# Performance work log

Hardware: AMD Instinct MI355X
Metric: run time of the kernel (lower is better)

Reference implementation:

```python
import jax, jax.numpy as jnp
import numpy as np

B, P, S, D = 256, 40, 60, 64


def setup_inputs() -> dict:
    key = jax.random.key(0)
    ks = jax.random.split(key, 12)
    sc = 1.0 / np.sqrt(D)
    return {
        "x": jax.random.normal(ks[0], (B, P, S, D), dtype=jnp.float32),
        "Wq": jax.random.normal(ks[1], (D, D), dtype=jnp.float32) * sc,
        "bq": jnp.zeros((D,), dtype=jnp.float32),
        "Wk": jax.random.normal(ks[2], (D, D), dtype=jnp.float32) * sc,
        "bk": jnp.zeros((D,), dtype=jnp.float32),
        "Wv": jax.random.normal(ks[3], (D, D), dtype=jnp.float32) * sc,
        "bv": jnp.zeros((D,), dtype=jnp.float32),
        "W1": jax.random.normal(ks[4], (D, D), dtype=jnp.float32) * sc,
        "b1": jnp.zeros((D,), dtype=jnp.float32),
        "W2": jax.random.normal(ks[5], (D, D), dtype=jnp.float32) * sc,
        "b2": jnp.zeros((D,), dtype=jnp.float32),
        "W3": jax.random.normal(ks[6], (1, D), dtype=jnp.float32) * sc,
        "b3": jnp.zeros((1,), dtype=jnp.float32),
    }


def reference(x, Wq, bq, Wk, bk, Wv, bv, W1, b1, W2, b2, W3, b3):
    # x: [B, P, S, D]; fully vectorized version of the per-batch torch loop
    q = jnp.einsum("bpsd,ed->bpse", x, Wq) + bq
    k = jnp.einsum("bpsd,ed->bpse", x, Wk) + bk
    v = jnp.einsum("bpsd,ed->bpse", x, Wv) + bv
    scores = jnp.einsum("bpqd,bpkd->bpqk", q, k) / jnp.sqrt(jnp.float32(D))
    attn = jax.nn.softmax(scores, axis=-1)
    weighted = jnp.einsum("bpqk,bpkd->bpqd", attn, v)  # [B,P,S,D]
    h = jax.nn.relu(jnp.einsum("bpsd,ed->bpse", weighted, W1) + b1)
    h = jax.nn.relu(jnp.einsum("bpsd,ed->bpse", h, W2) + b2)
    out = jnp.einsum("bpsd,od->bpso", h, W3) + b3  # [B,P,S,1]
    return out[..., 0]  # [B, P, S] == (B, NUM_PARTS, 60)
```

## Files before the change

kernel.cpp:

```cpp
#include <hip/hip_runtime.h>
#include <math.h>


typedef _Float16 half8 __attribute__((ext_vector_type(8)));
typedef __fp16 fp16x2 __attribute__((ext_vector_type(2)));
typedef float f4 __attribute__((ext_vector_type(4)));

#define MFMA16(a, b, c) __builtin_amdgcn_mfma_f32_16x16x32_f16((a), (b), (c), 0, 0, 0)

__global__ __launch_bounds__(256) void prep_weights(
    const float* __restrict__ Wq, const float* __restrict__ Wk,
    const float* __restrict__ Wv, const float* __restrict__ W1,
    const float* __restrict__ W2, _Float16* __restrict__ wsH) {
    int idx = blockIdx.x * 256 + threadIdx.x;
    int m = idx >> 12, r = idx & 4095;
    const float* src = (m == 0) ? Wq : (m == 1) ? Wk : (m == 2) ? Wv
                        : (m == 3) ? W1 : W2;
    float v;
    if (m < 3) {
        v = src[r];
    } else {
        int e = r >> 6, kp = r & 63;
        int ks = kp >> 5, gg = (kp >> 3) & 3, i = kp & 7;
        int d = 16 * (2 * ks + (i >> 2)) + 4 * gg + (i & 3);
        v = src[e * 64 + d];
    }
    wsH[idx] = (_Float16)v;
}

__device__ __forceinline__ half8 pk8(f4 a, f4 b) {
    union { half8 h; fp16x2 p[4]; } u;
    u.p[0] = __builtin_amdgcn_cvt_pkrtz(a[0], a[1]);
    u.p[1] = __builtin_amdgcn_cvt_pkrtz(a[2], a[3]);
    u.p[2] = __builtin_amdgcn_cvt_pkrtz(b[0], b[1]);
    u.p[3] = __builtin_amdgcn_cvt_pkrtz(b[2], b[3]);
    return u.h;
}

#define GEMM_H(AEXPR, BEXPR, CEXPR)                                          \
    do {                                                                     \
        _Pragma("unroll")                                                    \
        for (int ks = 0; ks < 2; ++ks) {                                     \
            half8 afr[4], bfr[2];                                            \
            _Pragma("unroll")                                                \
            for (int t = 0; t < 4; ++t) afr[t] = (AEXPR);                    \
            _Pragma("unroll")                                                \
            for (int nb = 0; nb < 2; ++nb) {                                 \
                const int nt = 2 * h + nb; (void)nt;                         \
                bfr[nb] = (BEXPR);                                           \
            }                                                                \
            _Pragma("unroll")                                                \
            for (int mt = 0; mt < 4; ++mt)                                   \
                _Pragma("unroll")                                            \
                for (int nb = 0; nb < 2; ++nb) {                             \
                    const int nt = 2 * h + nb; (void)nt;                     \
                    acc2[mt][nb] = MFMA16(afr[mt], bfr[nb],                  \
                                          ks == 0 ? (CEXPR) : acc2[mt][nb]); \
                }                                                            \
        }                                                                    \
    } while (0)

#define MKFR_H(dst, RELU)                                                    \
    do {                                                                     \
        _Pragma("unroll")                                                    \
        for (int nb = 0; nb < 2; ++nb)                                       \
            _Pragma("unroll")                                                \
            for (int ks = 0; ks < 2; ++ks) {                                 \
                f4 a_ = acc2[2 * ks][nb], b_ = acc2[2 * ks + 1][nb];         \
                if (RELU) {                                                  \
                    _Pragma("unroll")                                        \
                    for (int j = 0; j < 4; ++j) {                            \
                        a_[j] = fmaxf(a_[j], 0.f);                           \
                        b_[j] = fmaxf(b_[j], 0.f);                           \
                    }                                                        \
                }                                                            \
                dst[2 * h + nb][ks] = pk8(a_, b_);                           \
            }                                                                \
    } while (0)

#define WFRAG(widx, RB) (*(const half8*)&wlds[(widx) * 4096 + (16 * (RB) + lo) * 64 + \
                                              ((32 * ks + 8 * g) ^ ((lo & 7) << 3))])

#define XFRAG(RB) __extension__({                                            \
    int row_ = 16 * (RB) + lo;                                               \
    int rowc_ = row_ < 60 ? row_ : 48;                                       \
    half8 v_ = *(const half8*)&wlds[xbase + rowc_ * 64 +                     \
                                    ((32 * ks + 8 * g) ^ ((lo & 7) << 3))];  \
    if (row_ >= 60) { half8 z_ = {}; v_ = z_; }                              \
    v_; })

__global__ __launch_bounds__(512, 1) void fused_f16(
    const float* __restrict__ x, const _Float16* __restrict__ wH,
    const float* __restrict__ bq, const float* __restrict__ bk,
    const float* __restrict__ bv, const float* __restrict__ b1,
    const float* __restrict__ b2, const float* __restrict__ W3,
    const float* __restrict__ b3, float* __restrict__ out) {
    __shared__ __align__(16) _Float16 wlds[51200];

    const int tid = threadIdx.x;
    const int l = tid & 63;
    const int w = tid >> 6;
    const int lo = l & 15, g = l >> 4;

    #pragma unroll
    for (int rep = 0; rep < 5; ++rep) {
        int chunk = rep * 512 + tid;
        int widx = chunk >> 9;
        int rem = chunk & 511;
        int row = rem >> 3, c = rem & 7;
        *(half8*)&wlds[widx * 4096 + row * 64 + ((c * 8) ^ ((row & 7) << 3))] =
            *(const half8*)&wH[widx * 4096 + row * 64 + c * 8];
    }
    __syncthreads();

    const int part = blockIdx.x * 8 + w;
    const int xbase = 20480 + w * 3840;
    const float* __restrict__ xp = x + (size_t)part * (60 * 64);

    #pragma unroll
    for (int m = 0; m < 8; ++m) {
        int chunk = m * 64 + l;
        if (chunk < 480) {
            int row = chunk >> 3, c = chunk & 7;
            const float* p = xp + row * 64 + c * 8;
            half8 hv = pk8(*(const f4*)p, *(const f4*)(p + 4));
            *(half8*)&wlds[xbase + row * 64 + ((c * 8) ^ ((row & 7) << 3))] = hv;
        }
    }

    const f4 zc = {0.f, 0.f, 0.f, 0.f};
    f4 acc2[4][2];
    f4 brow[4];
    half8 qf[4][2], kf[4][2], vf[4][2], pf[4][2], wtf[4][2], h1f[4][2];

    #pragma unroll
    for (int mt = 0; mt < 4; ++mt) brow[mt] = *(const f4*)&bq[16 * mt + 4 * g];
    #pragma unroll
    for (int h = 0; h < 2; ++h) {
        GEMM_H(WFRAG(0, t), XFRAG(nt), brow[mt]);
        MKFR_H(qf, false);
    }

    #pragma unroll
    for (int mt = 0; mt < 4; ++mt) brow[mt] = *(const f4*)&bk[16 * mt + 4 * g];
    #pragma unroll
    for (int h = 0; h < 2; ++h) {
        GEMM_H(WFRAG(1, t), XFRAG(nt), brow[mt]);
        MKFR_H(kf, false);
    }

    #pragma unroll
    for (int h = 0; h < 2; ++h) {
        GEMM_H(kf[t][ks], qf[nt][ks], zc);
        #pragma unroll
        for (int nb = 0; nb < 2; ++nb) {
            float sum = 0.f;
            #pragma unroll
            for (int mt = 0; mt < 4; ++mt)
                #pragma unroll
                for (int j = 0; j < 4; ++j) {
                    float e = (mt == 3 && g == 3)
                                  ? 0.f
                                  : exp2f(acc2[mt][nb][j] * 0.1803368801111137f);
                    acc2[mt][nb][j] = e;
                    sum += e;
                }
            sum += __shfl_xor(sum, 16);
            sum += __shfl_xor(sum, 32);
            float inv = 1.f / sum;
            #pragma unroll
            for (int mt = 0; mt < 4; ++mt)
                #pragma unroll
                for (int j = 0; j < 4; ++j) acc2[mt][nb][j] *= inv;
        }
        MKFR_H(pf, false);
    }

    #pragma unroll
    for (int h = 0; h < 2; ++h) {
        float bc[2];
        #pragma unroll
        for (int nb = 0; nb < 2; ++nb) bc[nb] = bv[16 * (2 * h + nb) + lo];
        GEMM_H(XFRAG(t), WFRAG(2, nt),
               ((f4){bc[nb], bc[nb], bc[nb], bc[nb]}));
        MKFR_H(vf, false);
    }

    #pragma unroll
    for (int h = 0; h < 2; ++h) {
        GEMM_H(vf[t][ks], pf[nt][ks], zc);
        MKFR_H(wtf, false);
    }

    #pragma unroll
    for (int mt = 0; mt < 4; ++mt) brow[mt] = *(const f4*)&b1[16 * mt + 4 * g];
    #pragma unroll
    for (int h = 0; h < 2; ++h) {
        GEMM_H(WFRAG(3, t), wtf[nt][ks], brow[mt]);
        MKFR_H(h1f, true);
    }

    #pragma unroll
    for (int mt = 0; mt < 4; ++mt) brow[mt] = *(const f4*)&b2[16 * mt + 4 * g];
    f4 w3r[4];
    #pragma unroll
    for (int mt = 0; mt < 4; ++mt) w3r[mt] = *(const f4*)&W3[16 * mt + 4 * g];
    float b3v = b3[0];
    #pragma unroll
    for (int h = 0; h < 2; ++h) {
        GEMM_H(WFRAG(4, t), h1f[nt][ks], brow[mt]);
        #pragma unroll
        for (int nb = 0; nb < 2; ++nb) {
            float sres = 0.f;
            #pragma unroll
            for (int mt = 0; mt < 4; ++mt)
                #pragma unroll
                for (int j = 0; j < 4; ++j)
                    sres += fmaxf(acc2[mt][nb][j], 0.f) * w3r[mt][j];
            sres += __shfl_xor(sres, 16);
            sres += __shfl_xor(sres, 32);
            if (g == 0) {
                int s = 16 * (2 * h + nb) + lo;
                if (s < 60) out[(size_t)part * 60 + s] = sres + b3v;
            }
        }
    }
}

extern "C" void kernel_launch(void* const* d_in, const int* in_sizes, int n_in,
                              void* d_out, int out_size, void* d_ws, size_t ws_size,
                              hipStream_t stream) {
    const float* x  = (const float*)d_in[0];
    const float* Wq = (const float*)d_in[1];
    const float* bq = (const float*)d_in[2];
    const float* Wk = (const float*)d_in[3];
    const float* bk = (const float*)d_in[4];
    const float* Wv = (const float*)d_in[5];
    const float* bv = (const float*)d_in[6];
    const float* W1 = (const float*)d_in[7];
    const float* b1 = (const float*)d_in[8];
    const float* W2 = (const float*)d_in[9];
    const float* b2 = (const float*)d_in[10];
    const float* W3 = (const float*)d_in[11];
    const float* b3 = (const float*)d_in[12];
    _Float16* wsH = (_Float16*)d_ws;

    prep_weights<<<80, 256, 0, stream>>>(Wq, Wk, Wv, W1, W2, wsH);
    fused_f16<<<1280, 512, 0, stream>>>(x, wsH, bq, bk, bv, b1, b2, W3, b3,
                                        (float*)d_out);
}
```

Measured before the change: 69.92 us.

## Process two parts per wavefront to amortize weight loading and halve grid

Each wavefront now handles two (batch,part) slices instead of one, interleaving their MFMA chains so the two independent streams give instruction-level parallelism. The grid is halved to 640 blocks, so the per-block LDS weight staging is amortized over twice the work. LDS grows to 160KB and register pressure roughly doubles, which risks spills and leaves fewer blocks in flight on 256 CUs (640 blocks is about 2.5 waves).

Result: slower. 74.89 us (+7.1%).

```diff
diff --git a/kernel.cpp b/kernel.cpp
--- a/kernel.cpp
+++ b/kernel.cpp
@@ -37,7 +37,7 @@
     return u.h;
 }
 
-#define GEMM_H(AEXPR, BEXPR, CEXPR)                                          \
+#define GEMM_H(ACC, AEXPR, BEXPR, CEXPR)                                     \
     do {                                                                     \
         _Pragma("unroll")                                                    \
         for (int ks = 0; ks < 2; ++ks) {                                     \
@@ -54,19 +54,19 @@
                 _Pragma("unroll")                                            \
                 for (int nb = 0; nb < 2; ++nb) {                             \
                     const int nt = 2 * h + nb; (void)nt;                     \
-                    acc2[mt][nb] = MFMA16(afr[mt], bfr[nb],                  \
-                                          ks == 0 ? (CEXPR) : acc2[mt][nb]); \
+                    ACC[mt][nb] = MFMA16(afr[mt], bfr[nb],                   \
+                                         ks == 0 ? (CEXPR) : ACC[mt][nb]);   \
                 }                                                            \
         }                                                                    \
     } while (0)
 
-#define MKFR_H(dst, RELU)                                                    \
+#define MKFR_H(dst, ACC, RELU)                                               \
     do {                                                                     \
         _Pragma("unroll")                                                    \
         for (int nb = 0; nb < 2; ++nb)                                       \
             _Pragma("unroll")                                                \
             for (int ks = 0; ks < 2; ++ks) {                                 \
-                f4 a_ = acc2[2 * ks][nb], b_ = acc2[2 * ks + 1][nb];         \
+                f4 a_ = ACC[2 * ks][nb], b_ = ACC[2 * ks + 1][nb];           \
                 if (RELU) {                                                  \
                     _Pragma("unroll")                                        \
                     for (int j = 0; j < 4; ++j) {                            \
@@ -81,10 +81,10 @@
 #define WFRAG(widx, RB) (*(const half8*)&wlds[(widx) * 4096 + (16 * (RB) + lo) * 64 + \
                                               ((32 * ks + 8 * g) ^ ((lo & 7) << 3))])
 
-#define XFRAG(RB) __extension__({                                            \
+#define XFRAG(XB, RB) __extension__({                                        \
     int row_ = 16 * (RB) + lo;                                               \
     int rowc_ = row_ < 60 ? row_ : 48;                                       \
-    half8 v_ = *(const half8*)&wlds[xbase + rowc_ * 64 +                     \
+    half8 v_ = *(const half8*)&wlds[(XB) + rowc_ * 64 +                      \
                                     ((32 * ks + 8 * g) ^ ((lo & 7) << 3))];  \
     if (row_ >= 60) { half8 z_ = {}; v_ = z_; }                              \
     v_; })
@@ -95,7 +95,7 @@
     const float* __restrict__ bv, const float* __restrict__ b1,
     const float* __restrict__ b2, const float* __restrict__ W3,
     const float* __restrict__ b3, float* __restrict__ out) {
-    __shared__ __align__(16) _Float16 wlds[51200];
+    __shared__ __align__(16) _Float16 wlds[81920];
 
     const int tid = threadIdx.x;
     const int l = tid & 63;
@@ -113,92 +113,114 @@
     }
     __syncthreads();
 
-    const int part = blockIdx.x * 8 + w;
-    const int xbase = 20480 + w * 3840;
-    const float* __restrict__ xp = x + (size_t)part * (60 * 64);
-
-    #pragma unroll
-    for (int m = 0; m < 8; ++m) {
-        int chunk = m * 64 + l;
-        if (chunk < 480) {
-            int row = chunk >> 3, c = chunk & 7;
-            const float* p = xp + row * 64 + c * 8;
-            half8 hv = pk8(*(const f4*)p, *(const f4*)(p + 4));
-            *(half8*)&wlds[xbase + row * 64 + ((c * 8) ^ ((row & 7) << 3))] = hv;
+    const int pr0 = blockIdx.x * 16 + w * 2;
+    const int xb0 = 20480 + (2 * w + 0) * 3840;
+    const int xb1 = 20480 + (2 * w + 1) * 3840;
+
+    #pragma unroll
+    for (int P = 0; P < 2; ++P) {
+        const float* __restrict__ xp = x + (size_t)(pr0 + P) * (60 * 64);
+        const int XB = P ? xb1 : xb0;
+        #pragma unroll
+        for (int m = 0; m < 8; ++m) {
+            int chunk = m * 64 + l;
+            if (chunk < 480) {
+                int row = chunk >> 3, c = chunk & 7;
+                const float* p = xp + row * 64 + c * 8;
+                half8 hv = pk8(*(const f4*)p, *(const f4*)(p + 4));
+                *(half8*)&wlds[XB + row * 64 + ((c * 8) ^ ((row & 7) << 3))] = hv;
+            }
         }
     }
 
     const f4 zc = {0.f, 0.f, 0.f, 0.f};
-    f4 acc2[4][2];
+    f4 acc2[2][4][2];
     f4 brow[4];
-    half8 qf[4][2], kf[4][2], vf[4][2], pf[4][2], wtf[4][2], h1f[4][2];
+    half8 qf[2][4][2], kf[2][4][2], vf[2][4][2], pf[2][4][2], wtf[2][4][2],
+          h1f[2][4][2];
 
     #pragma unroll
     for (int mt = 0; mt < 4; ++mt) brow[mt] = *(const f4*)&bq[16 * mt + 4 * g];
     #pragma unroll
-    for (int h = 0; h < 2; ++h) {
-        GEMM_H(WFRAG(0, t), XFRAG(nt), brow[mt]);
-        MKFR_H(qf, false);
-    }
+    for (int h = 0; h < 2; ++h)
+        #pragma unroll
+        for (int P = 0; P < 2; ++P) {
+            const int XB = P ? xb1 : xb0;
+            GEMM_H(acc2[P], WFRAG(0, t), XFRAG(XB, nt), brow[mt]);
+            MKFR_H(qf[P], acc2[P], false);
+        }
 
     #pragma unroll
     for (int mt = 0; mt < 4; ++mt) brow[mt] = *(const f4*)&bk[16 * mt + 4 * g];
     #pragma unroll
-    for (int h = 0; h < 2; ++h) {
-        GEMM_H(WFRAG(1, t), XFRAG(nt), brow[mt]);
-        MKFR_H(kf, false);
-    }
-
-    #pragma unroll
-    for (int h = 0; h < 2; ++h) {
-        GEMM_H(kf[t][ks], qf[nt][ks], zc);
-        #pragma unroll
-        for (int nb = 0; nb < 2; ++nb) {
-            float sum = 0.f;
+    for (int h = 0; h < 2; ++h)
+        #pragma unroll
+        for (int P = 0; P < 2; ++P) {
+            const int XB = P ? xb1 : xb0;
+            GEMM_H(acc2[P], WFRAG(1, t), XFRAG(XB, nt), brow[mt]);
+            MKFR_H(kf[P], acc2[P], false);
+        }
+
+    #pragma unroll
+    for (int h = 0; h < 2; ++h)
+        #pragma unroll
+        for (int P = 0; P < 2; ++P) {
+            GEMM_H(acc2[P], kf[P][t][ks], qf[P][nt][ks], zc);
             #pragma unroll
-            for (int mt = 0; mt < 4; ++mt)
+            for (int nb = 0; nb < 2; ++nb) {
+                float sum = 0.f;
                 #pragma unroll
-                for (int j = 0; j < 4; ++j) {
-                    float e = (mt == 3 && g == 3)
-                                  ? 0.f
-                                  : exp2f(acc2[mt][nb][j] * 0.1803368801111137f);
-                    acc2[mt][nb][j] = e;
-                    sum += e;
-                }
-            sum += __shfl_xor(sum, 16);
-            sum += __shfl_xor(sum, 32);
-            float inv = 1.f / sum;
+                for (int mt = 0; mt < 4; ++mt)
+                    #pragma unroll
+                    for (int j = 0; j < 4; ++j) {
+                        float e = (mt == 3 && g == 3)
+                                      ? 0.f
+                                      : exp2f(acc2[P][mt][nb][j] *
+                                              0.1803368801111137f);
+                        acc2[P][mt][nb][j] = e;
+                        sum += e;
+                    }
+                sum += __shfl_xor(sum, 16);
+                sum += __shfl_xor(sum, 32);
+                float inv = 1.f / sum;
+                #pragma unroll
+                for (int mt = 0; mt < 4; ++mt)
+                    #pragma unroll
+                    for (int j = 0; j < 4; ++j) acc2[P][mt][nb][j] *= inv;
+            }
+            MKFR_H(pf[P], acc2[P], false);
+        }
+
+    #pragma unroll
+    for (int h = 0; h < 2; ++h)
+        #pragma unroll
+        for (int P = 0; P < 2; ++P) {
+            const int XB = P ? xb1 : xb0;
+            float bc[2];
             #pragma unroll
-            for (int mt = 0; mt < 4; ++mt)
-                #pragma unroll
-                for (int j = 0; j < 4; ++j) acc2[mt][nb][j] *= inv;
-        }
-        MKFR_H(pf, false);
-    }
-
-    #pragma unroll
-    for (int h = 0; h < 2; ++h) {
-        float bc[2];
-        #pragma unroll
-        for (int nb = 0; nb < 2; ++nb) bc[nb] = bv[16 * (2 * h + nb) + lo];
-        GEMM_H(XFRAG(t), WFRAG(2, nt),
-               ((f4){bc[nb], bc[nb], bc[nb], bc[nb]}));
-        MKFR_H(vf, false);
-    }
-
-    #pragma unroll
-    for (int h = 0; h < 2; ++h) {
-        GEMM_H(vf[t][ks], pf[nt][ks], zc);
-        MKFR_H(wtf, false);
-    }
+            for (int nb = 0; nb < 2; ++nb) bc[nb] = bv[16 * (2 * h + nb) + lo];
+            GEMM_H(acc2[P], XFRAG(XB, t), WFRAG(2, nt),
+                   ((f4){bc[nb], bc[nb], bc[nb], bc[nb]}));
+            MKFR_H(vf[P], acc2[P], false);
+        }
+
+    #pragma unroll
+    for (int h = 0; h < 2; ++h)
+        #pragma unroll
+        for (int P = 0; P < 2; ++P) {
+            GEMM_H(acc2[P], vf[P][t][ks], pf[P][nt][ks], zc);
+            MKFR_H(wtf[P], acc2[P], false);
+        }
 
     #pragma unroll
     for (int mt = 0; mt < 4; ++mt) brow[mt] = *(const f4*)&b1[16 * mt + 4 * g];
     #pragma unroll
-    for (int h = 0; h < 2; ++h) {
-        GEMM_H(WFRAG(3, t), wtf[nt][ks], brow[mt]);
-        MKFR_H(h1f, true);
-    }
+    for (int h = 0; h < 2; ++h)
+        #pragma unroll
+        for (int P = 0; P < 2; ++P) {
+            GEMM_H(acc2[P], WFRAG(3, t), wtf[P][nt][ks], brow[mt]);
+            MKFR_H(h1f[P], acc2[P], true);
+        }
 
     #pragma unroll
     for (int mt = 0; mt < 4; ++mt) brow[mt] = *(const f4*)&b2[16 * mt + 4 * g];
@@ -207,24 +229,26 @@
     for (int mt = 0; mt < 4; ++mt) w3r[mt] = *(const f4*)&W3[16 * mt + 4 * g];
     float b3v = b3[0];
     #pragma unroll
-    for (int h = 0; h < 2; ++h) {
-        GEMM_H(WFRAG(4, t), h1f[nt][ks], brow[mt]);
-        #pragma unroll
-        for (int nb = 0; nb < 2; ++nb) {
-            float sres = 0.f;
+    for (int h = 0; h < 2; ++h)
+        #pragma unroll
+        for (int P = 0; P < 2; ++P) {
+            GEMM_H(acc2[P], WFRAG(4, t), h1f[P][nt][ks], brow[mt]);
             #pragma unroll
-            for (int mt = 0; mt < 4; ++mt)
+            for (int nb = 0; nb < 2; ++nb) {
+                float sres = 0.f;
                 #pragma unroll
-                for (int j = 0; j < 4; ++j)
-                    sres += fmaxf(acc2[mt][nb][j], 0.f) * w3r[mt][j];
-            sres += __shfl_xor(sres, 16);
-            sres += __shfl_xor(sres, 32);
-            if (g == 0) {
-                int s = 16 * (2 * h + nb) + lo;
-                if (s < 60) out[(size_t)part * 60 + s] = sres + b3v;
+                for (int mt = 0; mt < 4; ++mt)
+                    #pragma unroll
+                    for (int j = 0; j < 4; ++j)
+                        sres += fmaxf(acc2[P][mt][nb][j], 0.f) * w3r[mt][j];
+                sres += __shfl_xor(sres, 16);
+                sres += __shfl_xor(sres, 32);
+                if (g == 0) {
+                    int s = 16 * (2 * h + nb) + lo;
+                    if (s < 60) out[(size_t)(pr0 + P) * 60 + s] = sres + b3v;
+                }
             }
         }
-    }
 }
 
 extern "C" void kernel_launch(void* const* d_in, const int* in_sizes, int n_in,
@@ -246,6 +270,6 @@
     _Float16* wsH = (_Float16*)d_ws;
 
     prep_weights<<<80, 256, 0, stream>>>(Wq, Wk, Wv, W1, W2, wsH);
-    fused_f16<<<1280, 512, 0, stream>>>(x, wsH, bq, bk, bv, b1, b2, W3, b3,
-                                        (float*)d_out);
-}
+    fused_f16<<<640, 512, 0, stream>>>(x, wsH, bq, bk, bv, b1, b2, W3, b3,
+                                       (float*)d_out);
+}
```

## Load x fragments directly into registers and drop LDS staging

Applied to the files above, without the earlier changes.

Removes the per-wave LDS staging of the x tile. Each lane now loads its MFMA fragments straight from global memory into registers, which shrinks shared memory from 100KB to 40KB. x is reloaded from global memory before the V projection, and an asm barrier keeps the compiler from holding the fragments live through the attention section, which limits register pressure. The trade-off is duplicated global reads: the fragment access pattern is less coalesced (32-byte pieces per lane), and the second read may or may not hit in cache.

After: 82.69 us. 18.3% more time.

```diff
diff --git a/kernel.cpp b/kernel.cpp
--- a/kernel.cpp
+++ b/kernel.cpp
@@ -37,6 +37,24 @@
     return u.h;
 }
 
+__device__ __forceinline__ void load_x(half8 xf[4][2], const float* __restrict__ xp,
+                                       int lo, int g) {
+    #pragma unroll
+    for (int t = 0; t < 4; ++t) {
+        int r = 16 * t + lo;
+        #pragma unroll
+        for (int ks = 0; ks < 2; ++ks) {
+            if (r < 60) {
+                const float* p = xp + r * 64 + ks * 32 + g * 8;
+                xf[t][ks] = pk8(*(const f4*)p, *(const f4*)(p + 4));
+            } else {
+                half8 z = {};
+                xf[t][ks] = z;
+            }
+        }
+    }
+}
+
 #define GEMM_H(AEXPR, BEXPR, CEXPR)                                          \
     do {                                                                     \
         _Pragma("unroll")                                                    \
@@ -81,21 +99,13 @@
 #define WFRAG(widx, RB) (*(const half8*)&wlds[(widx) * 4096 + (16 * (RB) + lo) * 64 + \
                                               ((32 * ks + 8 * g) ^ ((lo & 7) << 3))])
 
-#define XFRAG(RB) __extension__({                                            \
-    int row_ = 16 * (RB) + lo;                                               \
-    int rowc_ = row_ < 60 ? row_ : 48;                                       \
-    half8 v_ = *(const half8*)&wlds[xbase + rowc_ * 64 +                     \
-                                    ((32 * ks + 8 * g) ^ ((lo & 7) << 3))];  \
-    if (row_ >= 60) { half8 z_ = {}; v_ = z_; }                              \
-    v_; })
-
 __global__ __launch_bounds__(512, 1) void fused_f16(
     const float* __restrict__ x, const _Float16* __restrict__ wH,
     const float* __restrict__ bq, const float* __restrict__ bk,
     const float* __restrict__ bv, const float* __restrict__ b1,
     const float* __restrict__ b2, const float* __restrict__ W3,
     const float* __restrict__ b3, float* __restrict__ out) {
-    __shared__ __align__(16) _Float16 wlds[51200];
+    __shared__ __align__(16) _Float16 wlds[20480];
 
     const int tid = threadIdx.x;
     const int l = tid & 63;
@@ -114,30 +124,21 @@
     __syncthreads();
 
     const int part = blockIdx.x * 8 + w;
-    const int xbase = 20480 + w * 3840;
     const float* __restrict__ xp = x + (size_t)part * (60 * 64);
-
-    #pragma unroll
-    for (int m = 0; m < 8; ++m) {
-        int chunk = m * 64 + l;
-        if (chunk < 480) {
-            int row = chunk >> 3, c = chunk & 7;
-            const float* p = xp + row * 64 + c * 8;
-            half8 hv = pk8(*(const f4*)p, *(const f4*)(p + 4));
-            *(half8*)&wlds[xbase + row * 64 + ((c * 8) ^ ((row & 7) << 3))] = hv;
-        }
-    }
 
     const f4 zc = {0.f, 0.f, 0.f, 0.f};
     f4 acc2[4][2];
     f4 brow[4];
-    half8 qf[4][2], kf[4][2], vf[4][2], pf[4][2], wtf[4][2], h1f[4][2];
+    half8 xf[4][2], qf[4][2], kf[4][2], vf[4][2], pf[4][2], wtf[4][2],
+          h1f[4][2];
+
+    load_x(xf, xp, lo, g);
 
     #pragma unroll
     for (int mt = 0; mt < 4; ++mt) brow[mt] = *(const f4*)&bq[16 * mt + 4 * g];
     #pragma unroll
     for (int h = 0; h < 2; ++h) {
-        GEMM_H(WFRAG(0, t), XFRAG(nt), brow[mt]);
+        GEMM_H(WFRAG(0, t), xf[nt][ks], brow[mt]);
         MKFR_H(qf, false);
     }
 
@@ -145,7 +146,7 @@
     for (int mt = 0; mt < 4; ++mt) brow[mt] = *(const f4*)&bk[16 * mt + 4 * g];
     #pragma unroll
     for (int h = 0; h < 2; ++h) {
-        GEMM_H(WFRAG(1, t), XFRAG(nt), brow[mt]);
+        GEMM_H(WFRAG(1, t), xf[nt][ks], brow[mt]);
         MKFR_H(kf, false);
     }
 
@@ -176,12 +177,18 @@
         MKFR_H(pf, false);
     }
 
+    {
+        const float* xp2 = xp;
+        asm volatile("" : "+v"(xp2));
+        load_x(xf, xp2, lo, g);
+    }
+
     #pragma unroll
     for (int h = 0; h < 2; ++h) {
         float bc[2];
         #pragma unroll
         for (int nb = 0; nb < 2; ++nb) bc[nb] = bv[16 * (2 * h + nb) + lo];
-        GEMM_H(XFRAG(t), WFRAG(2, nt),
+        GEMM_H(xf[t][ks], WFRAG(2, nt),
                ((f4){bc[nb], bc[nb], bc[nb], bc[nb]}));
         MKFR_H(vf, false);
     }
```
